# Kernel tuning notes

Hardware: AMD Instinct MI355X
Metric: run time of the kernel (lower is better)

Reference implementation:

```python
import jax, jax.numpy as jnp
import numpy as np

N = 6144      # total residues (12 complexes x 512)
SEG = 512
NC = 14       # atom channels per residue
E = 64        # embed_size
HD = 128      # hidden_size
C = 25        # num_classes
K = 9         # k_neighbors
L = 3         # n_layers
ROUNDS = 3    # iter_round


def _forward(X, S, batch_id, embed, W_in, b_in, channel_w, eW1, eb1, eW2, eb2, cW1, cb1, cW2, cb2, nW1, nb1, nW2, nb2, mW1, mb1, mW2, mb2, oW1, ob1, oW2, ob2):
    n = X.shape[0]
    silu = jax.nn.silu
    # pairs in different complexes (or self) are never neighbors
    cross = (batch_id[:, None] != batch_id[None, :]) | jnp.eye(n, dtype=bool)
    Hmem = None
    H = None
    for t in range(ROUNDS):
        H0 = embed[S]                                    # residue embedding [N,E]
        if Hmem is not None:                             # keep_memory: memory_ffn(H_prev)
            m = silu(Hmem) @ mW1 + mb1
            H0 = H0 + (silu(m) @ mW2 + mb2)
        H = H0 @ W_in + b_in                             # [N,HD]
        # dynamic KNN edge construction on current CA coordinates (_knn_edges)
        ca = X[:, 1]                                     # [N,3]
        d2 = jnp.sum((ca[:, None, :] - ca[None, :, :]) ** 2, -1)
        d2 = jnp.where(cross, 1e9, d2)
        _, nbr = jax.lax.top_k(-d2, K)                   # [N,K] neighbor indices
        for l in range(L):                               # AMEGNN / AMEncoder layers
            Hj = H[nbr]                                  # gather [N,K,HD]
            Xj = X[nbr]                                  # gather [N,K,NC,3]
            diff = X[:, None] - Xj                       # [N,K,NC,3]
            # channel-weighted radial feature
            radial = jnp.einsum('nkcd,nkcd,c->nk', diff, diff, channel_w)[..., None]
            Hi = jnp.broadcast_to(H[:, None], Hj.shape)
            ein = jnp.concatenate([Hi, Hj, radial], -1)  # [N,K,2HD+1]
            msg = silu(silu(ein @ eW1[l] + eb1[l]) @ eW2[l] + eb2[l])
            scale = silu(msg @ cW1[l] + cb1[l]) @ cW2[l] + cb2[l]     # [N,K,1]
            X = X + jnp.mean(diff * scale[..., None], axis=1)        # equivariant coord update
            agg = jnp.sum(msg, axis=1)                   # scatter-sum over neighbors [N,HD]
            H = H + silu(jnp.concatenate([H, agg], -1) @ nW1[l] + nb1[l]) @ nW2[l] + nb2[l]
        Hmem = H
    logits = silu(silu(H) @ oW1 + ob1) @ oW2 + ob2       # ffn_residue
    return logits, X


def setup_inputs() -> dict:
    key = jax.random.key(0)
    ks = jax.random.split(key, 16)
    r = lambda i, shape, s=0.05: jax.random.normal(ks[i], shape, dtype=jnp.float32) * s
    return {
        'X': jax.random.normal(ks[0], (N, NC, 3), dtype=jnp.float32) * 3.0,
        'S': jax.random.randint(ks[1], (N,), 0, C),
        'batch_id': jnp.arange(N, dtype=jnp.int32) // SEG,
        'embed': r(2, (C, E), 1.0),
        'W_in': r(3, (E, HD)), 'b_in': jnp.zeros((HD,), jnp.float32),
        'channel_w': jax.random.uniform(ks[4], (NC,), dtype=jnp.float32),
        'eW1': r(5, (L, 2 * HD + 1, HD)), 'eb1': jnp.zeros((L, HD), jnp.float32),
        'eW2': r(6, (L, HD, HD)), 'eb2': jnp.zeros((L, HD), jnp.float32),
        'cW1': r(7, (L, HD, HD)), 'cb1': jnp.zeros((L, HD), jnp.float32),
        'cW2': r(8, (L, HD, 1)), 'cb2': jnp.zeros((L, 1), jnp.float32),
        'nW1': r(9, (L, 2 * HD, HD)), 'nb1': jnp.zeros((L, HD), jnp.float32),
        'nW2': r(10, (L, HD, HD)), 'nb2': jnp.zeros((L, HD), jnp.float32),
        'mW1': r(11, (HD, HD)), 'mb1': jnp.zeros((HD,), jnp.float32),
        'mW2': r(12, (HD, E)), 'mb2': jnp.zeros((E,), jnp.float32),
        'oW1': r(13, (HD, HD)), 'ob1': jnp.zeros((HD,), jnp.float32),
        'oW2': r(14, (HD, C)), 'ob2': jnp.zeros((C,), jnp.float32),
    }


def reference(X, S, batch_id, embed, W_in, b_in, channel_w, eW1, eb1, eW2, eb2, cW1, cb1, cW2, cb2, nW1, nb1, nW2, nb2, mW1, mb1, mW2, mb2, oW1, ob1, oW2, ob2):
    return _forward(X, S, batch_id, embed, W_in, b_in, channel_w, eW1, eb1, eW2, eb2, cW1, cb1, cW2, cb2, nW1, nb1, nW2, nb2, mW1, mb1, mW2, mb2, oW1, ob1, oW2, ob2)
```

## Files before the change

### kernel.cpp

```cpp
#include <hip/hip_runtime.h>
#include <math.h>

#define NNODE 6144
#define SEG   512
#define NCH   14
#define XD    42
#define ED    64
#define HD    128
#define NCLS  25
#define KN    9
#define NPB   7
#define ROWS  64
#define EDGE_BLOCKS ((NNODE + NPB - 1) / NPB)

typedef __attribute__((ext_vector_type(8))) short short8;
typedef __attribute__((ext_vector_type(4))) short short4v;
typedef __attribute__((ext_vector_type(4))) float f32x4;

__device__ __forceinline__ float silu_f(float x) {
  return x / (1.0f + __expf(-x));
}
__device__ __forceinline__ short f2bf(float x) {
  unsigned u = __builtin_bit_cast(unsigned, x);
  unsigned r = (u + 0x7fffu + ((u >> 16) & 1u)) >> 16;
  return (short)r;
}
__device__ __forceinline__ float bf2f(short s) {
  unsigned u = ((unsigned)(unsigned short)s) << 16;
  return __builtin_bit_cast(float, u);
}
__device__ __forceinline__ f32x4 mfma16(short8 a, short8 b, f32x4 c) {
  return __builtin_amdgcn_mfma_f32_16x16x32_bf16(a, b, c, 0, 0, 0);
}
__device__ __forceinline__ int swz128(int row, int col) {
  return row * 128 + (col ^ ((row & 7) << 3));
}
__device__ __forceinline__ int swz256(int row, int col) {
  return row * 256 + (col ^ ((row & 7) << 3));
}

__global__ __launch_bounds__(256) void prep_weights(
    const float* __restrict__ eW1, const float* __restrict__ eW2,
    const float* __restrict__ cW1, const float* __restrict__ nW1,
    const float* __restrict__ nW2, short* __restrict__ out)
{
  const int mat = blockIdx.y % 5, l = blockIdx.y / 5;
  const int idx = blockIdx.x * 256 + threadIdx.x;
  const int K = (mat == 0 || mat == 3) ? 256 : 128;
  if (idx >= K * 128) return;
  const int n = idx / K, k = idx - n * K;
  const float* src;
  switch (mat) {
    case 0: src = eW1 + (size_t)l * 257 * 128; break;
    case 1: src = eW2 + (size_t)l * 128 * 128; break;
    case 2: src = cW1 + (size_t)l * 128 * 128; break;
    case 3: src = nW1 + (size_t)l * 256 * 128; break;
    default: src = nW2 + (size_t)l * 128 * 128; break;
  }
  const int dofs[5] = {0, 32768, 49152, 65536, 98304};
  out[(size_t)l * 114688 + dofs[mat] + idx] = f2bf(src[k * 128 + n]);
}

__global__ void copy_kernel(const float* __restrict__ src, float* __restrict__ dst, int n) {
  int i = blockIdx.x * blockDim.x + threadIdx.x;
  if (i < n) dst[i] = src[i];
}

__global__ __launch_bounds__(512) void pq_kernel(
    const float* __restrict__ Hin, const short* __restrict__ W1T,
    float* __restrict__ PQ)
{
  __shared__ __align__(16) short A[32 * HD];
  const int t = threadIdx.x;
  const int m0 = blockIdx.x * 32;

  const float4* H4 = (const float4*)(Hin + (size_t)m0 * HD);
  for (int idx = t; idx < 32 * 32; idx += 512) {
    const int r = idx >> 5, c4 = idx & 31;
    float4 v = H4[r * 32 + c4];
    short4v s;
    s.x = f2bf(v.x); s.y = f2bf(v.y); s.z = f2bf(v.z); s.w = f2bf(v.w);
    *(short4v*)&A[swz128(r, c4 * 4)] = s;
  }
  __syncthreads();

  const int wid = t >> 6, lane = t & 63;
  const int lr = lane & 15, lk = lane >> 4;
  const int mt = wid >> 2;
  const int nb = (wid & 3) * 4;
  const int rA = mt * 16 + lr;

  f32x4 acc[4] = {};
#pragma unroll
  for (int ks = 0; ks < 4; ++ks) {
    const int k0 = ks * 32 + lk * 8;
    const short8 a = *(const short8*)&A[swz128(rA, k0)];
#pragma unroll
    for (int ni = 0; ni < 4; ++ni) {
      const int c = (nb + ni) * 16 + lr;
      const short* bp = (c < HD) ? (W1T + c * 256 + k0)
                                 : (W1T + (c - HD) * 256 + HD + k0);
      const short8 b = *(const short8*)bp;
      acc[ni] = mfma16(a, b, acc[ni]);
    }
  }
#pragma unroll
  for (int ni = 0; ni < 4; ++ni) {
    const int c = (nb + ni) * 16 + lr;
#pragma unroll
    for (int g = 0; g < 4; ++g) {
      const int row = mt * 16 + lk * 4 + g;
      PQ[(size_t)(m0 + row) * 256 + c] = acc[ni][g];
    }
  }
}

__global__ __launch_bounds__(128) void h_init_kernel(
    const float* __restrict__ embed, const int* __restrict__ S,
    const float* __restrict__ W_in, const float* __restrict__ b_in,
    const float* __restrict__ Hmem,
    const float* __restrict__ mW1, const float* __restrict__ mb1,
    const float* __restrict__ mW2, const float* __restrict__ mb2,
    float* __restrict__ Hout)
{
  __shared__ float a1[HD];
  __shared__ float a2[HD];
  __shared__ float h0[ED];
  const int i = blockIdx.x, j = threadIdx.x;

  if (Hmem) {
    a1[j] = silu_f(Hmem[i * HD + j]);
    __syncthreads();
    float m0 = 0.f, m1 = 0.f, m2 = 0.f, m3 = 0.f;
    for (int k = 0; k < HD; k += 4) {
      m0 = fmaf(a1[k + 0], mW1[(k + 0) * HD + j], m0);
      m1 = fmaf(a1[k + 1], mW1[(k + 1) * HD + j], m1);
      m2 = fmaf(a1[k + 2], mW1[(k + 2) * HD + j], m2);
      m3 = fmaf(a1[k + 3], mW1[(k + 3) * HD + j], m3);
    }
    a2[j] = silu_f(mb1[j] + ((m0 + m1) + (m2 + m3)));
    __syncthreads();
    if (j < ED) {
      float v0 = 0.f, v1 = 0.f, v2 = 0.f, v3 = 0.f;
      for (int k = 0; k < HD; k += 4) {
        v0 = fmaf(a2[k + 0], mW2[(k + 0) * ED + j], v0);
        v1 = fmaf(a2[k + 1], mW2[(k + 1) * ED + j], v1);
        v2 = fmaf(a2[k + 2], mW2[(k + 2) * ED + j], v2);
        v3 = fmaf(a2[k + 3], mW2[(k + 3) * ED + j], v3);
      }
      h0[j] = embed[S[i] * ED + j] + mb2[j] + ((v0 + v1) + (v2 + v3));
    }
  } else {
    if (j < ED) h0[j] = embed[S[i] * ED + j];
  }
  __syncthreads();
  float h0a = 0.f, h1a = 0.f, h2a = 0.f, h3a = 0.f;
  for (int k = 0; k < ED; k += 4) {
    h0a = fmaf(h0[k + 0], W_in[(k + 0) * HD + j], h0a);
    h1a = fmaf(h0[k + 1], W_in[(k + 1) * HD + j], h1a);
    h2a = fmaf(h0[k + 2], W_in[(k + 2) * HD + j], h2a);
    h3a = fmaf(h0[k + 3], W_in[(k + 3) * HD + j], h3a);
  }
  Hout[i * HD + j] = b_in[j] + ((h0a + h1a) + (h2a + h3a));
}

__global__ __launch_bounds__(256) void knn_kernel(const float* __restrict__ X,
                                                  int* __restrict__ nbr)
{
  const int w = threadIdx.x >> 6, lane = threadIdx.x & 63;
  const int i = blockIdx.x * 4 + w;
  const int base = (i / SEG) * SEG;

  const float cx = X[i * XD + 3], cy = X[i * XD + 4], cz = X[i * XD + 5];
  float dv[8];
  int   di[8];
#pragma unroll
  for (int q = 0; q < 8; ++q) {
    const int j = base + lane + q * 64;
    float dx = __fsub_rn(cx, X[j * XD + 3]);
    float dy = __fsub_rn(cy, X[j * XD + 4]);
    float dz = __fsub_rn(cz, X[j * XD + 5]);
    float d2 = __fadd_rn(__fadd_rn(__fmul_rn(dx, dx), __fmul_rn(dy, dy)), __fmul_rn(dz, dz));
    if (j == i) d2 = 1e9f;
    dv[q] = d2; di[q] = j;
  }
  for (int it = 0; it < KN; ++it) {
    float bv = dv[0]; int bi = di[0];
#pragma unroll
    for (int q = 1; q < 8; ++q)
      if (dv[q] < bv || (dv[q] == bv && di[q] < bi)) { bv = dv[q]; bi = di[q]; }
#pragma unroll
    for (int m = 1; m < 64; m <<= 1) {
      float ov = __shfl_xor(bv, m, 64);
      int   oi = __shfl_xor(bi, m, 64);
      if (ov < bv || (ov == bv && oi < bi)) { bv = ov; bi = oi; }
    }
    if (lane == 0) nbr[i * KN + it] = bi;
    const int rel = bi - base;
    const int oq = rel >> 6;
#pragma unroll
    for (int q = 0; q < 8; ++q)
      if (q == oq && (rel & 63) == lane) dv[q] = 3e38f;
  }
}

__global__ __launch_bounds__(512) void edge_layer_kernel(
    const float* __restrict__ Hin,  float* __restrict__ Hout,
    const float* __restrict__ Xin,  float* __restrict__ Xout,
    const int*   __restrict__ nbr,  const float* __restrict__ channel_w,
    const float* __restrict__ PQ,
    const float* __restrict__ eW1,  const float* __restrict__ eb1,
    const float* __restrict__ eb2,  const float* __restrict__ cb1,
    const float* __restrict__ cW2,  const float* __restrict__ cb2,
    const float* __restrict__ nb1,  const float* __restrict__ nb2,
    const short* __restrict__ W2T,  const short* __restrict__ C1T,
    const short* __restrict__ N1T,  const short* __restrict__ N2T)
{
  __shared__ __align__(16) short bufA[ROWS * HD];
  __shared__ __align__(16) short bufB[ROWS * HD];
  __shared__ __align__(16) short nodeA[16 * 256];
  __shared__ __align__(16) short uT[16 * HD];
  __shared__ float XiS[NPB][XD];
  __shared__ float radialS[ROWS];
  __shared__ float scaleS[ROWS];
  __shared__ int   nbrS[ROWS];

  const int t  = threadIdx.x;
  const int n0 = blockIdx.x * NPB;
  const int nvalid = (NNODE - n0 < NPB) ? (NNODE - n0) : NPB;
  const int evalid = nvalid * KN;

  if (t < ROWS) {
    const int j = (t < evalid) ? nbr[n0 * KN + t] : n0;
    nbrS[t] = j;
    float r = 0.f;
    if (t < evalid) {
      const int nd = t / KN;
      const float* xi = Xin + (size_t)(n0 + nd) * XD;
      const float* xj = Xin + (size_t)j * XD;
#pragma unroll
      for (int c = 0; c < NCH; ++c) {
        float dx = xi[c * 3 + 0] - xj[c * 3 + 0];
        float dy = xi[c * 3 + 1] - xj[c * 3 + 1];
        float dz = xi[c * 3 + 2] - xj[c * 3 + 2];
        r += channel_w[c] * (dx * dx + dy * dy + dz * dz);
      }
    }
    radialS[t] = r;
  }
  {
    float* XiSf = &XiS[0][0];
    for (int idx = t; idx < NPB * XD; idx += 512) {
      const int nd = idx / XD;
      XiSf[idx] = (nd < nvalid) ? Xin[n0 * XD + idx] : 0.f;
    }
  }
  __syncthreads();

  {
    const float4* PQ4 = (const float4*)PQ;
    const float4* w2564 = (const float4*)(eW1 + 256 * HD);
    const float4* eb14 = (const float4*)eb1;
    for (int idx = t; idx < ROWS * (HD / 4); idx += 512) {
      const int row = idx >> 5, c4 = idx & 31;
      const int nd = row / KN;
      const int inode = n0 + ((nd < nvalid) ? nd : 0);
      const int jnode = nbrS[row];
      const float4 p = PQ4[(size_t)inode * 64 + c4];
      const float4 q = PQ4[(size_t)jnode * 64 + 32 + c4];
      const float rad = radialS[row];
      const float4 w = w2564[c4];
      const float4 bb = eb14[c4];
      short4v s;
      s.x = f2bf(silu_f(p.x + q.x + rad * w.x + bb.x));
      s.y = f2bf(silu_f(p.y + q.y + rad * w.y + bb.y));
      s.z = f2bf(silu_f(p.z + q.z + rad * w.z + bb.z));
      s.w = f2bf(silu_f(p.w + q.w + rad * w.w + bb.w));
      *(short4v*)&bufA[swz128(row, c4 * 4)] = s;
    }
  }
  __syncthreads();

  const int wid  = t >> 6;
  const int lane = t & 63;
  const int m2 = wid >> 2;
  const int n2 = wid & 3;
  const int lr = lane & 15;
  const int lk = lane >> 4;
  const int rA0 = (m2 * 2) * 16 + lr;
  const int rA1 = rA0 + 16;

  {
    f32x4 acc[2][2] = {};
    const short* b0p = W2T + ((n2 * 2) * 16 + lr) * 128;
    const short* b1p = b0p + 16 * 128;
#pragma unroll
    for (int ks = 0; ks < 4; ++ks) {
      const int k0 = ks * 32 + lk * 8;
      const short8 a0 = *(const short8*)&bufA[swz128(rA0, k0)];
      const short8 a1 = *(const short8*)&bufA[swz128(rA1, k0)];
      const short8 b0 = *(const short8*)(b0p + k0);
      const short8 b1 = *(const short8*)(b1p + k0);
      acc[0][0] = mfma16(a0, b0, acc[0][0]);
      acc[0][1] = mfma16(a0, b1, acc[0][1]);
      acc[1][0] = mfma16(a1, b0, acc[1][0]);
      acc[1][1] = mfma16(a1, b1, acc[1][1]);
    }
#pragma unroll
    for (int ni = 0; ni < 2; ++ni) {
      const int col = (n2 * 2 + ni) * 16 + lr;
      const float bias = eb2[col];
#pragma unroll
      for (int mi = 0; mi < 2; ++mi) {
        const int rb = (m2 * 2 + mi) * 16 + lk * 4;
#pragma unroll
        for (int g = 0; g < 4; ++g)
          bufB[swz128(rb + g, col)] = f2bf(silu_f(acc[mi][ni][g] + bias));
      }
    }
  }
  __syncthreads();

  {
    f32x4 acc[2][2] = {};
    const short* b0p = C1T + ((n2 * 2) * 16 + lr) * 128;
    const short* b1p = b0p + 16 * 128;
#pragma unroll
    for (int ks = 0; ks < 4; ++ks) {
      const int k0 = ks * 32 + lk * 8;
      const short8 a0 = *(const short8*)&bufB[swz128(rA0, k0)];
      const short8 a1 = *(const short8*)&bufB[swz128(rA1, k0)];
      const short8 b0 = *(const short8*)(b0p + k0);
      const short8 b1 = *(const short8*)(b1p + k0);
      acc[0][0] = mfma16(a0, b0, acc[0][0]);
      acc[0][1] = mfma16(a0, b1, acc[0][1]);
      acc[1][0] = mfma16(a1, b0, acc[1][0]);
      acc[1][1] = mfma16(a1, b1, acc[1][1]);
    }
#pragma unroll
    for (int ni = 0; ni < 2; ++ni) {
      const int col = (n2 * 2 + ni) * 16 + lr;
      const float bias = cb1[col];
#pragma unroll
      for (int mi = 0; mi < 2; ++mi) {
        const int rb = (m2 * 2 + mi) * 16 + lk * 4;
#pragma unroll
        for (int g = 0; g < 4; ++g)
          bufA[swz128(rb + g, col)] = f2bf(silu_f(acc[mi][ni][g] + bias));
      }
    }
  }
  __syncthreads();

  {
    const int row = t >> 3, part = t & 7;
    float s = 0.f;
#pragma unroll
    for (int qq = 0; qq < 16; ++qq) {
      const int k = part * 16 + qq;
      s = fmaf(bf2f(bufA[swz128(row, k)]), cW2[k], s);
    }
    s += __shfl_xor(s, 1, 64);
    s += __shfl_xor(s, 2, 64);
    s += __shfl_xor(s, 4, 64);
    if (part == 0) scaleS[row] = s + cb2[0];
  }
  for (int idx = t; idx < 16 * 256; idx += 512) {
    const int r = idx >> 8, c = idx & 255;
    float v = 0.f;
    if (r < nvalid) {
      if (c < HD) v = Hin[(size_t)(n0 + r) * HD + c];
      else {
        const int col = c - HD;
#pragma unroll
        for (int k = 0; k < KN; ++k) v += bf2f(bufB[swz128(r * KN + k, col)]);
      }
    }
    nodeA[swz256(r, c)] = f2bf(v);
  }
  __syncthreads();

  {
    f32x4 acc = {};
    const short* bp = N1T + (wid * 16 + lr) * 256;
#pragma unroll
    for (int ks = 0; ks < 8; ++ks) {
      const int k0 = ks * 32 + lk * 8;
      const short8 a = *(const short8*)&nodeA[swz256(lr, k0)];
      const short8 b = *(const short8*)(bp + k0);
      acc = mfma16(a, b, acc);
    }
    const int col = wid * 16 + lr;
    const float bias = nb1[col];
#pragma unroll
    for (int g = 0; g < 4; ++g)
      uT[swz128(lk * 4 + g, col)] = f2bf(silu_f(acc[g] + bias));
  }
  {
    float* XiSf = &XiS[0][0];
    for (int idx = t; idx < NPB * XD; idx += 512) {
      const int nd = idx / XD, e = idx - nd * XD;
      if (nd < nvalid) {
        const float xi = XiSf[idx];
        float a = 0.f;
#pragma unroll
        for (int k = 0; k < KN; ++k) {
          const int r = nd * KN + k;
          a += (xi - Xin[(size_t)nbrS[r] * XD + e]) * scaleS[r];
        }
        Xout[(size_t)(n0 + nd) * XD + e] = xi + a / 9.0f;
      }
    }
  }
  __syncthreads();

  {
    f32x4 acc = {};
    const short* bp = N2T + (wid * 16 + lr) * 128;
#pragma unroll
    for (int ks = 0; ks < 4; ++ks) {
      const int k0 = ks * 32 + lk * 8;
      const short8 a = *(const short8*)&uT[swz128(lr, k0)];
      const short8 b = *(const short8*)(bp + k0);
      acc = mfma16(a, b, acc);
    }
    const int col = wid * 16 + lr;
    const float bias = nb2[col];
#pragma unroll
    for (int g = 0; g < 4; ++g) {
      const int row = lk * 4 + g;
      if (row < nvalid)
        Hout[(size_t)(n0 + row) * HD + col] =
            Hin[(size_t)(n0 + row) * HD + col] + acc[g] + bias;
    }
  }
}

__global__ __launch_bounds__(128) void out_kernel(
    const float* __restrict__ H, const float* __restrict__ X,
    const float* __restrict__ oW1, const float* __restrict__ ob1,
    const float* __restrict__ oW2, const float* __restrict__ ob2,
    float* __restrict__ out)
{
  __shared__ float hs[HD];
  __shared__ float u[HD];
  const int i = blockIdx.x, j = threadIdx.x;

  hs[j] = silu_f(H[i * HD + j]);
  __syncthreads();
  float a0 = 0.f, a1 = 0.f, a2 = 0.f, a3 = 0.f;
  for (int k = 0; k < HD; k += 4) {
    a0 = fmaf(hs[k + 0], oW1[(k + 0) * HD + j], a0);
    a1 = fmaf(hs[k + 1], oW1[(k + 1) * HD + j], a1);
    a2 = fmaf(hs[k + 2], oW1[(k + 2) * HD + j], a2);
    a3 = fmaf(hs[k + 3], oW1[(k + 3) * HD + j], a3);
  }
  u[j] = silu_f(ob1[j] + ((a0 + a1) + (a2 + a3)));
  __syncthreads();
  if (j < NCLS) {
    float o0 = 0.f, o1 = 0.f, o2 = 0.f, o3 = 0.f;
    for (int k = 0; k < HD; k += 4) {
      o0 = fmaf(u[k + 0], oW2[(k + 0) * NCLS + j], o0);
      o1 = fmaf(u[k + 1], oW2[(k + 1) * NCLS + j], o1);
      o2 = fmaf(u[k + 2], oW2[(k + 2) * NCLS + j], o2);
      o3 = fmaf(u[k + 3], oW2[(k + 3) * NCLS + j], o3);
    }
    out[i * NCLS + j] = ob2[j] + ((o0 + o1) + (o2 + o3));
  }
  if (j < XD) out[NNODE * NCLS + i * XD + j] = X[i * XD + j];
}

extern "C" void kernel_launch(void* const* d_in, const int* in_sizes, int n_in,
                              void* d_out, int out_size, void* d_ws, size_t ws_size,
                              hipStream_t stream)
{
  const float* X0       = (const float*)d_in[0];
  const int*   S        = (const int*)  d_in[1];
  const float* embed    = (const float*)d_in[3];
  const float* W_in     = (const float*)d_in[4];
  const float* b_in     = (const float*)d_in[5];
  const float* channelw = (const float*)d_in[6];
  const float* eW1      = (const float*)d_in[7];
  const float* eb1      = (const float*)d_in[8];
  const float* eW2      = (const float*)d_in[9];
  const float* eb2      = (const float*)d_in[10];
  const float* cW1      = (const float*)d_in[11];
  const float* cb1      = (const float*)d_in[12];
  const float* cW2      = (const float*)d_in[13];
  const float* cb2      = (const float*)d_in[14];
  const float* nW1      = (const float*)d_in[15];
  const float* nb1      = (const float*)d_in[16];
  const float* nW2      = (const float*)d_in[17];
  const float* nb2      = (const float*)d_in[18];
  const float* mW1      = (const float*)d_in[19];
  const float* mb1      = (const float*)d_in[20];
  const float* mW2      = (const float*)d_in[21];
  const float* mb2      = (const float*)d_in[22];
  const float* oW1      = (const float*)d_in[23];
  const float* ob1      = (const float*)d_in[24];
  const float* oW2      = (const float*)d_in[25];
  const float* ob2      = (const float*)d_in[26];

  char* ws = (char*)d_ws;
  const size_t HBYTES = (size_t)NNODE * HD * sizeof(float);
  const size_t XBYTES = (size_t)NNODE * XD * sizeof(float);
  float* Hb[2] = { (float*)(ws), (float*)(ws + HBYTES) };
  float* Xb[2] = { (float*)(ws + 2 * HBYTES), (float*)(ws + 2 * HBYTES + XBYTES) };
  int*   nbr   = (int*)(ws + 2 * HBYTES + 2 * XBYTES);
  short* Wbf   = (short*)(ws + 2 * HBYTES + 2 * XBYTES + (size_t)NNODE * KN * sizeof(int));
  float* PQ    = (float*)(ws + 2 * HBYTES + 2 * XBYTES + (size_t)NNODE * KN * sizeof(int)
                             + 3 * 114688 * sizeof(short));

  prep_weights<<<dim3(128, 15), 256, 0, stream>>>(eW1, eW2, cW1, nW1, nW2, Wbf);
  copy_kernel<<<(NNODE * XD + 255) / 256, 256, 0, stream>>>(X0, Xb[0], NNODE * XD);

  int hc = 0, xc = 0;
  for (int t = 0; t < 3; ++t) {
    const float* Hmem = (t == 0) ? nullptr : Hb[hc];
    h_init_kernel<<<NNODE, HD, 0, stream>>>(embed, S, W_in, b_in, Hmem,
                                            mW1, mb1, mW2, mb2, Hb[hc ^ 1]);
    hc ^= 1;
    knn_kernel<<<NNODE / 4, 256, 0, stream>>>(Xb[xc], nbr);
    for (int l = 0; l < 3; ++l) {
      const short* Wl = Wbf + (size_t)l * 114688;
      pq_kernel<<<NNODE / 32, 512, 0, stream>>>(Hb[hc], Wl, PQ);
      edge_layer_kernel<<<EDGE_BLOCKS, 512, 0, stream>>>(
          Hb[hc], Hb[hc ^ 1], Xb[xc], Xb[xc ^ 1], nbr, channelw, PQ,
          eW1 + (size_t)l * 257 * HD, eb1 + (size_t)l * HD,
          eb2 + (size_t)l * HD,  cb1 + (size_t)l * HD,
          cW2 + (size_t)l * HD,  cb2 + (size_t)l,
          nb1 + (size_t)l * HD,  nb2 + (size_t)l * HD,
          Wl + 32768, Wl + 49152, Wl + 65536, Wl + 98304);
      hc ^= 1; xc ^= 1;
    }
  }
  out_kernel<<<NNODE, HD, 0, stream>>>(Hb[hc], Xb[xc], oW1, ob1, oW2, ob2, (float*)d_out);
}
```

Measured before the change: 666.3 us.

## Shrink edge-kernel LDS, parallelize radial computation, merge first sync phase

Node-level LDS buffers are cut from 16 rows to NPB rows, with MFMA A-operand loads and outputs masked to valid rows, and launch_bounds asks for more resident blocks. The radial feature is now computed by 8 threads per edge row with a shuffle reduction instead of 64 threads looping over 14 channels. This removes the radialS buffer and one __syncthreads, and the Hin half of nodeA is staged early. The aim is higher occupancy and less serial prologue work, at the cost of possible register pressure from the occupancy hint.

```diff
diff --git a/kernel.cpp b/kernel.cpp
--- a/kernel.cpp
+++ b/kernel.cpp
@@ -204,7 +204,7 @@
   }
 }
 
-__global__ __launch_bounds__(512) void edge_layer_kernel(
+__global__ __launch_bounds__(512, 8) void edge_layer_kernel(
     const float* __restrict__ Hin,  float* __restrict__ Hout,
     const float* __restrict__ Xin,  float* __restrict__ Xout,
     const int*   __restrict__ nbr,  const float* __restrict__ channel_w,
@@ -218,10 +218,9 @@
 {
   __shared__ __align__(16) short bufA[ROWS * HD];
   __shared__ __align__(16) short bufB[ROWS * HD];
-  __shared__ __align__(16) short nodeA[16 * 256];
-  __shared__ __align__(16) short uT[16 * HD];
+  __shared__ __align__(16) short nodeA[NPB * 256];
+  __shared__ __align__(16) short uT[NPB * HD];
   __shared__ float XiS[NPB][XD];
-  __shared__ float radialS[ROWS];
   __shared__ float scaleS[ROWS];
   __shared__ int   nbrS[ROWS];
 
@@ -230,52 +229,66 @@
   const int nvalid = (NNODE - n0 < NPB) ? (NNODE - n0) : NPB;
   const int evalid = nvalid * KN;
 
-  if (t < ROWS) {
-    const int j = (t < evalid) ? nbr[n0 * KN + t] : n0;
-    nbrS[t] = j;
+  {
+    const int row  = t >> 3;
+    const int part = t & 7;
+    const bool rvalid = row < evalid;
+    const int nd = row / KN;
+    const int jn = rvalid ? nbr[n0 * KN + row] : n0;
+    if (part == 0) nbrS[row] = jn;
+
     float r = 0.f;
-    if (t < evalid) {
-      const int nd = t / KN;
+    if (rvalid) {
       const float* xi = Xin + (size_t)(n0 + nd) * XD;
-      const float* xj = Xin + (size_t)j * XD;
-#pragma unroll
-      for (int c = 0; c < NCH; ++c) {
+      const float* xj = Xin + (size_t)jn * XD;
+      {
+        const int c = part;
         float dx = xi[c * 3 + 0] - xj[c * 3 + 0];
         float dy = xi[c * 3 + 1] - xj[c * 3 + 1];
         float dz = xi[c * 3 + 2] - xj[c * 3 + 2];
         r += channel_w[c] * (dx * dx + dy * dy + dz * dz);
       }
-    }
-    radialS[t] = r;
-  }
-  {
-    float* XiSf = &XiS[0][0];
-    for (int idx = t; idx < NPB * XD; idx += 512) {
-      const int nd = idx / XD;
-      XiSf[idx] = (nd < nvalid) ? Xin[n0 * XD + idx] : 0.f;
-    }
-  }
-  __syncthreads();
-
-  {
+      if (part < 6) {
+        const int c = part + 8;
+        float dx = xi[c * 3 + 0] - xj[c * 3 + 0];
+        float dy = xi[c * 3 + 1] - xj[c * 3 + 1];
+        float dz = xi[c * 3 + 2] - xj[c * 3 + 2];
+        r += channel_w[c] * (dx * dx + dy * dy + dz * dz);
+      }
+    }
+    r += __shfl_xor(r, 1, 64);
+    r += __shfl_xor(r, 2, 64);
+    r += __shfl_xor(r, 4, 64);
+
+    {
+      float* XiSf = &XiS[0][0];
+      for (int idx = t; idx < NPB * XD; idx += 512) {
+        const int nd2 = idx / XD;
+        XiSf[idx] = (nd2 < nvalid) ? Xin[n0 * XD + idx] : 0.f;
+      }
+      for (int idx = t; idx < NPB * HD; idx += 512) {
+        const int r2 = idx >> 7, c = idx & 127;
+        const float v = (r2 < nvalid) ? Hin[(size_t)(n0 + r2) * HD + c] : 0.f;
+        nodeA[swz256(r2, c)] = f2bf(v);
+      }
+    }
+
+    const int inode = n0 + ((nd < nvalid) ? nd : 0);
     const float4* PQ4 = (const float4*)PQ;
     const float4* w2564 = (const float4*)(eW1 + 256 * HD);
     const float4* eb14 = (const float4*)eb1;
-    for (int idx = t; idx < ROWS * (HD / 4); idx += 512) {
-      const int row = idx >> 5, c4 = idx & 31;
-      const int nd = row / KN;
-      const int inode = n0 + ((nd < nvalid) ? nd : 0);
-      const int jnode = nbrS[row];
+#pragma unroll
+    for (int ii = 0; ii < 4; ++ii) {
+      const int c4 = part + ii * 8;
       const float4 p = PQ4[(size_t)inode * 64 + c4];
-      const float4 q = PQ4[(size_t)jnode * 64 + 32 + c4];
-      const float rad = radialS[row];
+      const float4 q = PQ4[(size_t)jn * 64 + 32 + c4];
       const float4 w = w2564[c4];
       const float4 bb = eb14[c4];
       short4v s;
-      s.x = f2bf(silu_f(p.x + q.x + rad * w.x + bb.x));
-      s.y = f2bf(silu_f(p.y + q.y + rad * w.y + bb.y));
-      s.z = f2bf(silu_f(p.z + q.z + rad * w.z + bb.z));
-      s.w = f2bf(silu_f(p.w + q.w + rad * w.w + bb.w));
+      s.x = f2bf(silu_f(p.x + q.x + r * w.x + bb.x));
+      s.y = f2bf(silu_f(p.y + q.y + r * w.y + bb.y));
+      s.z = f2bf(silu_f(p.z + q.z + r * w.z + bb.z));
+      s.w = f2bf(silu_f(p.w + q.w + r * w.w + bb.w));
       *(short4v*)&bufA[swz128(row, c4 * 4)] = s;
     }
   }
@@ -365,18 +378,14 @@
     s += __shfl_xor(s, 4, 64);
     if (part == 0) scaleS[row] = s + cb2[0];
   }
-  for (int idx = t; idx < 16 * 256; idx += 512) {
-    const int r = idx >> 8, c = idx & 255;
+  for (int idx = t; idx < NPB * HD; idx += 512) {
+    const int r2 = idx >> 7, col = idx & 127;
     float v = 0.f;
-    if (r < nvalid) {
-      if (c < HD) v = Hin[(size_t)(n0 + r) * HD + c];
-      else {
-        const int col = c - HD;
-#pragma unroll
-        for (int k = 0; k < KN; ++k) v += bf2f(bufB[swz128(r * KN + k, col)]);
-      }
-    }
-    nodeA[swz256(r, c)] = f2bf(v);
+    if (r2 < nvalid) {
+#pragma unroll
+      for (int k = 0; k < KN; ++k) v += bf2f(bufB[swz128(r2 * KN + k, col)]);
+    }
+    nodeA[swz256(r2, col + HD)] = f2bf(v);
   }
   __syncthreads();
 
@@ -386,15 +395,18 @@
 #pragma unroll
     for (int ks = 0; ks < 8; ++ks) {
       const int k0 = ks * 32 + lk * 8;
-      const short8 a = *(const short8*)&nodeA[swz256(lr, k0)];
+      short8 a = {0, 0, 0, 0, 0, 0, 0, 0};
+      if (lr < NPB) a = *(const short8*)&nodeA[swz256(lr, k0)];
       const short8 b = *(const short8*)(bp + k0);
       acc = mfma16(a, b, acc);
     }
     const int col = wid * 16 + lr;
     const float bias = nb1[col];
 #pragma unroll
-    for (int g = 0; g < 4; ++g)
-      uT[swz128(lk * 4 + g, col)] = f2bf(silu_f(acc[g] + bias));
+    for (int g = 0; g < 4; ++g) {
+      const int orow = lk * 4 + g;
+      if (orow < NPB) uT[swz128(orow, col)] = f2bf(silu_f(acc[g] + bias));
+    }
   }
   {
     float* XiSf = &XiS[0][0];
@@ -420,7 +432,8 @@
 #pragma unroll
     for (int ks = 0; ks < 4; ++ks) {
       const int k0 = ks * 32 + lk * 8;
-      const short8 a = *(const short8*)&uT[swz128(lr, k0)];
+      short8 a = {0, 0, 0, 0, 0, 0, 0, 0};
+      if (lr < NPB) a = *(const short8*)&uT[swz128(lr, k0)];
       const short8 b = *(const short8*)(bp + k0);
       acc = mfma16(a, b, acc);
     }
```

Result: faster. 610.1 us (-8.4%).
